# Kernel optimization log

Hardware: AMD Instinct MI355X
Metric: run time of the kernel (lower is better)

## Reference

```python
import jax, jax.numpy as jnp
import numpy as np

TI, N, TO, D, H, FF, V, L = 128, 8, 32, 512, 8, 2048, 2000, 6


def _ln(x, s, b, eps=1e-5):
    m = jnp.mean(x, -1, keepdims=True)
    v = jnp.var(x, -1, keepdims=True)
    return (x - m) / jnp.sqrt(v + eps) * s + b


def _pos_enc(t, d):
    pos = np.arange(t)[:, None]
    div = np.exp(np.arange(0, d, 2) * (-np.log(10000.0) / d))
    pe = np.zeros((t, d), np.float32)
    pe[:, 0::2] = np.sin(pos * div)
    pe[:, 1::2] = np.cos(pos * div)
    return jnp.asarray(pe)


def _forward(enc_out, embed, enc_w, enc_b, qkv_w, qkv_b, o_w, o_b, ln1_s, ln1_b,
             ff1_w, ff1_b, ff2_w, ff2_b, ln2_s, ln2_b, out_w, tgt_pad, tgt_len, sos):
    n, to = tgt_pad.shape
    t = to + 1
    v, d = embed.shape
    hd = d // H
    # prepend <sos>, embed (scaled) + sinusoidal positions; dropout omitted (eval)
    tgt = jnp.pad(tgt_pad, ((0, 0), (1, 0)), constant_values=sos)  # N x T
    x = embed[tgt] * jnp.sqrt(jnp.float32(d)) + _pos_enc(t, d)[None]  # N x T x D
    x = x.transpose(1, 0, 2)  # T x N x D (time-major, pytorch default)
    causal = jnp.triu(jnp.ones((t, t), bool), k=1)  # True = masked
    lens = jnp.maximum(tgt_len, 1)
    pad = jnp.arange(t)[None, :] >= lens[:, None]  # N x T key padding
    mask = causal[None, None] | pad[:, None, None, :]
    neg = jnp.float32(-1e9)

    def heads(z):  # T x N x D -> N x H x T x hd
        return z.reshape(t, n, H, hd).transpose(1, 2, 0, 3)

    for l in range(L):  # post-norm TransformerEncoderLayer, relu FFN
        qkv = jnp.einsum('tnd,ed->tne', x, qkv_w[l]) + qkv_b[l]
        q, k_, v_ = jnp.split(qkv, 3, axis=-1)
        q = heads(q) / jnp.sqrt(jnp.float32(hd))
        k_, v_ = heads(k_), heads(v_)
        sc = jnp.einsum('nhqd,nhkd->nhqk', q, k_)
        att = jax.nn.softmax(jnp.where(mask, neg, sc), axis=-1)
        o = jnp.einsum('nhqk,nhkd->nhqd', att, v_).transpose(2, 0, 1, 3).reshape(t, n, d)
        o = jnp.einsum('tnd,ed->tne', o, o_w[l]) + o_b[l]
        x = _ln(x + o, ln1_s[l], ln1_b[l])
        h = jax.nn.relu(jnp.einsum('tnd,fd->tnf', x, ff1_w[l]) + ff1_b[l])
        h = jnp.einsum('tnf,df->tnd', h, ff2_w[l]) + ff2_b[l]
        x = _ln(x + h, ln2_s[l], ln2_b[l])

    enc = jnp.einsum('ind,ed->ine', enc_out, enc_w) + enc_b  # Ti x N x D
    add = jnp.tanh(enc[None] + x[:, None])  # (To+1) x Ti x N x D joiner
    out = jnp.einsum('tind,vd->tinv', add, out_w)  # (To+1) x Ti x N x V
    return out.transpose(2, 1, 0, 3)  # N x Ti x (To+1) x V


def setup_inputs() -> dict:
    key = jax.random.key(0)
    ks = jax.random.split(key, 12)
    s = 0.02
    return dict(
        enc_out=jax.random.normal(ks[0], (TI, N, D), jnp.float32),
        embed=jax.random.normal(ks[1], (V, D), jnp.float32) * s,
        enc_w=jax.random.normal(ks[2], (D, D), jnp.float32) * s,
        enc_b=jnp.zeros((D,), jnp.float32),
        qkv_w=jax.random.normal(ks[3], (L, 3 * D, D), jnp.float32) * s,
        qkv_b=jnp.zeros((L, 3 * D), jnp.float32),
        o_w=jax.random.normal(ks[4], (L, D, D), jnp.float32) * s,
        o_b=jnp.zeros((L, D), jnp.float32),
        ln1_s=jnp.ones((L, D), jnp.float32),
        ln1_b=jnp.zeros((L, D), jnp.float32),
        ff1_w=jax.random.normal(ks[5], (L, FF, D), jnp.float32) * s,
        ff1_b=jnp.zeros((L, FF), jnp.float32),
        ff2_w=jax.random.normal(ks[6], (L, D, FF), jnp.float32) * s,
        ff2_b=jnp.zeros((L, D), jnp.float32),
        ln2_s=jnp.ones((L, D), jnp.float32),
        ln2_b=jnp.zeros((L, D), jnp.float32),
        out_w=jax.random.normal(ks[7], (V, D), jnp.float32) * s,
        tgt_pad=jax.random.randint(ks[8], (N, TO), 0, V),
        tgt_len=jax.random.randint(ks[9], (N,), TO // 2, TO + 2),
        sos=1,
    )


def reference(enc_out, embed, enc_w, enc_b, qkv_w, qkv_b, o_w, o_b, ln1_s, ln1_b,
              ff1_w, ff1_b, ff2_w, ff2_b, ln2_s, ln2_b, out_w, tgt_pad, tgt_len, sos):
    return _forward(enc_out, embed, enc_w, enc_b, qkv_w, qkv_b, o_w, o_b, ln1_s, ln1_b,
                    ff1_w, ff1_b, ff2_w, ff2_b, ln2_s, ln2_b, out_w, tgt_pad, tgt_len, sos)
```

## Files before the change

### kernel.cpp

```cpp
#include <hip/hip_runtime.h>
#include <hip/hip_bf16.h>
#include <math.h>

#define TI 128
#define NB 8
#define TO 32
#define TT 33
#define D 512
#define NH 8
#define HD 64
#define FF 2048
#define V 2000
#define NL 6
#define NTOK (TT*NB)
#define MJ (NB*TI*TT)
#define GRID 256

typedef __attribute__((ext_vector_type(4))) float  f4;
typedef __attribute__((ext_vector_type(8))) short  shortx8;
typedef unsigned short u16;

static constexpr size_t QO = 0;
static constexpr size_t OO = 4718592;
static constexpr size_t F1 = 6291456;
static constexpr size_t F2 = 12582912;
static constexpr size_t EW = 18874368;

__device__ __forceinline__ u16 f2bf(float f) {
    unsigned u = __float_as_uint(f);
    unsigned r = (u + 0x7fffu + ((u >> 16) & 1u)) >> 16;
    return (u16)r;
}
__device__ __forceinline__ float bf2f(u16 h) {
    return __uint_as_float(((unsigned)h) << 16);
}
__device__ __forceinline__ float wsum(float v) {
#pragma unroll
    for (int off = 32; off; off >>= 1) v += __shfl_xor(v, off, 64);
    return v;
}
__device__ __forceinline__ float wmax(float v) {
#pragma unroll
    for (int off = 32; off; off >>= 1) v = fmaxf(v, __shfl_xor(v, off, 64));
    return v;
}
__device__ __forceinline__ f4 mfma16(shortx8 a, shortx8 b, f4 c) {
    return __builtin_amdgcn_mfma_f32_16x16x32_bf16(a, b, c, 0, 0, 0);
}
__device__ __forceinline__ void async16(const void* g, void* l) {
    __builtin_amdgcn_global_load_lds(
        (const __attribute__((address_space(1))) unsigned int*)g,
        (__attribute__((address_space(3))) unsigned int*)l, 16, 0, 0);
}

__device__ __forceinline__ void grid_sync(unsigned gs, unsigned xcc, unsigned nblk,
                                          unsigned* gbar, unsigned* xarr,
                                          unsigned* xdn)
{
    __syncthreads();
    if (threadIdx.x == 0) {
        unsigned a = __hip_atomic_fetch_add(&xarr[xcc * 16], 1u, __ATOMIC_RELAXED,
                                            __HIP_MEMORY_SCOPE_AGENT);
        bool leader = (a == gs * nblk - 1);
        if (leader)
            asm volatile("buffer_wbl2 sc1\n\ts_waitcnt vmcnt(0)" ::: "memory");
        __hip_atomic_fetch_add(gbar, 1u, __ATOMIC_RELAXED, __HIP_MEMORY_SCOPE_AGENT);
        unsigned tgt = (gs + 1) * (unsigned)GRID;
        while (__hip_atomic_load(gbar, __ATOMIC_RELAXED,
                                 __HIP_MEMORY_SCOPE_AGENT) < tgt)
            __builtin_amdgcn_s_sleep(2);
        if (leader) {
            asm volatile("buffer_inv sc1\n\ts_waitcnt vmcnt(0)" ::: "memory");
            __hip_atomic_fetch_add(&xdn[xcc * 16], 1u, __ATOMIC_RELAXED,
                                   __HIP_MEMORY_SCOPE_AGENT);
        } else {
            while (__hip_atomic_load(&xdn[xcc * 16], __ATOMIC_RELAXED,
                                     __HIP_MEMORY_SCOPE_AGENT) < gs)
                __builtin_amdgcn_s_sleep(2);
            asm volatile("buffer_inv sc0\n\ts_waitcnt vmcnt(0)" ::: "memory");
        }
    }
    __syncthreads();
}

__global__ __launch_bounds__(256) void fused_convert(
    const float* __restrict__ qw, const float* __restrict__ ow,
    const float* __restrict__ f1w, const float* __restrict__ f2w,
    const float* __restrict__ ew, u16* __restrict__ Wh, u16* __restrict__ Wl,
    const float* __restrict__ enc_out, u16* __restrict__ eh, u16* __restrict__ el,
    const float* __restrict__ emb, const int* __restrict__ tgt_pad,
    const int* __restrict__ sos, float* __restrict__ x,
    u16* __restrict__ xh, u16* __restrict__ xl, unsigned* __restrict__ bar)
{
    const int bid = blockIdx.x, tid = threadIdx.x;
    if (bid == 0) { bar[tid] = 0; bar[tid + 256] = 0; }
    if (bid < 18688) {
        int i4 = bid * 256 + tid;
        const float* src; int loc;
        if (i4 < 1179648)      { src = qw;  loc = i4; }
        else if (i4 < 1572864) { src = ow;  loc = i4 - 1179648; }
        else if (i4 < 3145728) { src = f1w; loc = i4 - 1572864; }
        else if (i4 < 4718592) { src = f2w; loc = i4 - 3145728; }
        else                   { src = ew;  loc = i4 - 4718592; }
        f4 v = *(const f4*)(src + (size_t)loc * 4);
        ushort4 h, l;
        h.x = f2bf(v[0]); l.x = f2bf(v[0] - bf2f(h.x));
        h.y = f2bf(v[1]); l.y = f2bf(v[1] - bf2f(h.y));
        h.z = f2bf(v[2]); l.z = f2bf(v[2] - bf2f(h.z));
        h.w = f2bf(v[3]); l.w = f2bf(v[3] - bf2f(h.w));
        *(ushort4*)(Wh + (size_t)i4 * 4) = h;
        *(ushort4*)(Wl + (size_t)i4 * 4) = l;
    } else if (bid < 19200) {
        int i = (bid - 18688) * 256 + tid;
        f4 v = *(const f4*)(enc_out + (size_t)i * 4);
        ushort4 h, l;
        h.x = f2bf(v[0]); l.x = f2bf(v[0] - bf2f(h.x));
        h.y = f2bf(v[1]); l.y = f2bf(v[1] - bf2f(h.y));
        h.z = f2bf(v[2]); l.z = f2bf(v[2] - bf2f(h.z));
        h.w = f2bf(v[3]); l.w = f2bf(v[3] - bf2f(h.w));
        *(ushort4*)(eh + (size_t)i * 4) = h;
        *(ushort4*)(el + (size_t)i * 4) = l;
    } else {
        int idx = (bid - 19200) * 256 + tid;
        if (idx < NTOK * D) {
            int d = idx & (D - 1);
            int row = idx >> 9;
            int t = row >> 3, n = row & 7;
            int tok = (t == 0) ? *sos : tgt_pad[n * TO + t - 1];
            float freq = __expf((float)(d & ~1) * (-0.017988946039015984f));
            float ang = (float)t * freq;
            float pe = (d & 1) ? cosf(ang) : sinf(ang);
            float v = emb[tok * D + d] * 22.627416997969522f + pe;
            x[idx] = v;
            u16 h = f2bf(v);
            xh[idx] = h;
            xl[idx] = f2bf(v - bf2f(h));
        }
    }
}

template<int MODE>
__device__ void gemm_tile(
    u16 (*ls)[4][2048], int mt, int nt, int zz,
    const u16* __restrict__ Ah, const u16* __restrict__ Al, int lda,
    const u16* __restrict__ Bh, const u16* __restrict__ Bl, int ldb,
    const float* __restrict__ bias,
    float* __restrict__ C, u16* __restrict__ Ch, u16* __restrict__ Cl,
    int M, int ldc, int ksteps)
{
    const int tid = threadIdx.x, lane = tid & 63, w = tid >> 6;
    const int wr = (w >> 1) * 32, wc = (w & 1) * 32;
    const int m0 = mt * 64, n0 = nt * 64;
    const int qd = lane >> 4, mm = lane & 15;
    const int kb = (MODE == 1) ? zz * ksteps * 32 : 0;
    f4 acc[2][2] = {};
    const u16* Ab  = Ah + (size_t)m0 * lda + kb;
    const u16* Alb = Al + (size_t)m0 * lda + kb;
    const u16* Bb  = Bh + (size_t)n0 * ldb + kb;
    const u16* Blb = Bl + (size_t)n0 * ldb + kb;
    const int srow = tid >> 2;
    const int sc8  = ((tid & 3) ^ (srow & 3)) * 8;

    auto stage = [&](int b, int it) {
        int k0 = it * 32;
        async16(Ab  + (size_t)srow * lda + k0 + sc8, &ls[b][0][tid * 8]);
        async16(Alb + (size_t)srow * lda + k0 + sc8, &ls[b][1][tid * 8]);
        async16(Bb  + (size_t)srow * ldb + k0 + sc8, &ls[b][2][tid * 8]);
        async16(Blb + (size_t)srow * ldb + k0 + sc8, &ls[b][3][tid * 8]);
    };

    stage(0, 0);
    if (ksteps > 1) stage(1, 1);
    for (int it = 0; it < ksteps; ++it) {
        if (it + 1 < ksteps) asm volatile("s_waitcnt vmcnt(4)" ::: "memory");
        else                 asm volatile("s_waitcnt vmcnt(0)" ::: "memory");
        __builtin_amdgcn_s_barrier();
        if (it + 2 < ksteps) stage((it + 2) % 3, it + 2);
        const int cur = it % 3;
        shortx8 aH[2], aL[2], bH[2], bL[2];
#pragma unroll
        for (int rt = 0; rt < 2; ++rt) {
            int row = wr + rt * 16 + mm;
            int ca = (qd ^ (row & 3)) * 8;
            aH[rt] = *(const shortx8*)&ls[cur][0][row * 32 + ca];
            aL[rt] = *(const shortx8*)&ls[cur][1][row * 32 + ca];
            int col = wc + rt * 16 + mm;
            int cb = (qd ^ (col & 3)) * 8;
            bH[rt] = *(const shortx8*)&ls[cur][2][col * 32 + cb];
            bL[rt] = *(const shortx8*)&ls[cur][3][col * 32 + cb];
        }
#pragma unroll
        for (int rt = 0; rt < 2; ++rt)
#pragma unroll
            for (int ct = 0; ct < 2; ++ct) {
                acc[rt][ct] = mfma16(aH[rt], bH[ct], acc[rt][ct]);
                acc[rt][ct] = mfma16(aH[rt], bL[ct], acc[rt][ct]);
                acc[rt][ct] = mfma16(aL[rt], bH[ct], acc[rt][ct]);
            }
    }
    float* Cz = C;
    if (MODE == 1) Cz = C + (size_t)zz * (size_t)M * ldc;
#pragma unroll
    for (int rt = 0; rt < 2; ++rt)
#pragma unroll
        for (int ct = 0; ct < 2; ++ct)
#pragma unroll
            for (int reg = 0; reg < 4; ++reg) {
                int grow = m0 + wr + rt * 16 + qd * 4 + reg;
                int gcol = n0 + wc + ct * 16 + mm;
                if (grow < M) {
                    float v = acc[rt][ct][reg];
                    if (MODE != 1) v += bias[gcol];
                    if (MODE == 2) {
                        v = fmaxf(v, 0.f);
                        u16 h = f2bf(v);
                        Ch[(size_t)grow * ldc + gcol] = h;
                        Cl[(size_t)grow * ldc + gcol] = f2bf(v - bf2f(h));
                    } else {
                        Cz[(size_t)grow * ldc + gcol] = v;
                    }
                }
            }
}

__device__ void attn_body(u16* lsr, int bid,
                          const float* __restrict__ qkv,
                          const int* __restrict__ tgt_len,
                          u16* __restrict__ oh, u16* __restrict__ ol)
{
    const int n = bid >> 3, h = bid & 7;
    const int tid = threadIdx.x, lane = tid & 63, w = tid >> 6;
    float* sq  = (float*)lsr;
    float* skT = sq + TT * HD;
    float* sv  = skT + HD * TT;
    for (int idx = tid; idx < TT * HD; idx += 256) {
        int t = idx >> 6, d = idx & 63;
        size_t base = (size_t)(t * NB + n) * (3 * D) + h * HD + d;
        sq[idx] = qkv[base] * 0.125f;
        skT[d * TT + t] = qkv[base + D];
        sv[idx] = qkv[base + 2 * D];
    }
    int len = max(tgt_len[n], 1);
    __syncthreads();
    for (int r = w; r < TT; r += 4) {
        bool ok = (lane < TT) && (lane <= r) && (lane < len);
        float s = -INFINITY;
        if (ok) {
            float dot = 0.f;
#pragma unroll 8
            for (int d = 0; d < HD; ++d) dot += sq[r * HD + d] * skT[d * TT + lane];
            s = dot;
        }
        float mx = wmax(s);
        float e = ok ? __expf(s - mx) : 0.f;
        float sum = wsum(e);
        float att = e / sum;
        float o = 0.f;
#pragma unroll
        for (int k = 0; k < TT; ++k) {
            float a = __shfl(att, k, 64);
            o += a * sv[k * HD + lane];
        }
        size_t oi = (size_t)(r * NB + n) * D + h * HD + lane;
        u16 hv = f2bf(o);
        oh[oi] = hv;
        ol[oi] = f2bf(o - bf2f(hv));
    }
}

template<int NP, int BIAS>
__device__ void add_ln_body(int bid,
    float* __restrict__ x, const float* __restrict__ r,
    const float* __restrict__ bias2,
    const float* __restrict__ s, const float* __restrict__ b,
    u16* __restrict__ xh, u16* __restrict__ xl)
{
    int row = bid * 4 + (threadIdx.x >> 6);
    int lane = threadIdx.x & 63;
    if (row >= NTOK) return;
    float* xr = x + (size_t)row * D;
    f4 v1 = *(const f4*)(xr + lane * 4);
    f4 v2 = *(const f4*)(xr + 256 + lane * 4);
#pragma unroll
    for (int p = 0; p < NP; ++p) {
        const float* rr = r + (size_t)p * (NTOK * D) + (size_t)row * D;
        v1 += *(const f4*)(rr + lane * 4);
        v2 += *(const f4*)(rr + 256 + lane * 4);
    }
    if (BIAS) {
        v1 += *(const f4*)(bias2 + lane * 4);
        v2 += *(const f4*)(bias2 + 256 + lane * 4);
    }
    float sum = 0.f, sq = 0.f;
#pragma unroll
    for (int j = 0; j < 4; ++j) {
        sum += v1[j] + v2[j];
        sq += v1[j] * v1[j] + v2[j] * v2[j];
    }
    sum = wsum(sum); sq = wsum(sq);
    float mean = sum * (1.f / D);
    float var = sq * (1.f / D) - mean * mean;
    float rstd = rsqrtf(var + 1e-5f);
    f4 o1, o2;
    ushort4 h1, l1, h2, l2;
    u16 th, tl;
#pragma unroll
    for (int j = 0; j < 4; ++j) {
        int c1 = lane * 4 + j, c2 = c1 + 256;
        o1[j] = (v1[j] - mean) * rstd * s[c1] + b[c1];
        o2[j] = (v2[j] - mean) * rstd * s[c2] + b[c2];
    }
    th = f2bf(o1[0]); tl = f2bf(o1[0] - bf2f(th)); h1.x = th; l1.x = tl;
    th = f2bf(o1[1]); tl = f2bf(o1[1] - bf2f(th)); h1.y = th; l1.y = tl;
    th = f2bf(o1[2]); tl = f2bf(o1[2] - bf2f(th)); h1.z = th; l1.z = tl;
    th = f2bf(o1[3]); tl = f2bf(o1[3] - bf2f(th)); h1.w = th; l1.w = tl;
    th = f2bf(o2[0]); tl = f2bf(o2[0] - bf2f(th)); h2.x = th; l2.x = tl;
    th = f2bf(o2[1]); tl = f2bf(o2[1] - bf2f(th)); h2.y = th; l2.y = tl;
    th = f2bf(o2[2]); tl = f2bf(o2[2] - bf2f(th)); h2.z = th; l2.z = tl;
    th = f2bf(o2[3]); tl = f2bf(o2[3] - bf2f(th)); h2.w = th; l2.w = tl;
    *(f4*)(xr + lane * 4) = o1;
    *(f4*)(xr + 256 + lane * 4) = o2;
    *(ushort4*)(xh + (size_t)row * D + lane * 4) = h1;
    *(ushort4*)(xl + (size_t)row * D + lane * 4) = l1;
    *(ushort4*)(xh + (size_t)row * D + 256 + lane * 4) = h2;
    *(ushort4*)(xl + (size_t)row * D + 256 + lane * 4) = l2;
}

__global__ __launch_bounds__(256, 1) void decoder_coop(
    const u16* __restrict__ Wh, const u16* __restrict__ Wl,
    const float* __restrict__ qkv_b, const float* __restrict__ o_b,
    const float* __restrict__ ln1_s, const float* __restrict__ ln1_b,
    const float* __restrict__ ff1_b, const float* __restrict__ ff2_b,
    const float* __restrict__ ln2_s, const float* __restrict__ ln2_b,
    const float* __restrict__ enc_b, const int* __restrict__ tgt_len,
    float* __restrict__ x, float* __restrict__ qkvb,
    float* __restrict__ part, float* __restrict__ encb,
    u16* __restrict__ xh, u16* __restrict__ xl,
    u16* __restrict__ oh, u16* __restrict__ ol,
    u16* __restrict__ hh, u16* __restrict__ hl,
    const u16* __restrict__ eh, const u16* __restrict__ el,
    unsigned* __restrict__ bar)
{
    __shared__ u16 ls[3][4][2048];
    const int bid = blockIdx.x;
    const int tid = threadIdx.x;

    unsigned xcc;
    asm("s_getreg_b32 %0, hwreg(HW_REG_XCC_ID, 0, 4)" : "=s"(xcc));
    xcc &= 7;
    unsigned* gbar = bar;
    unsigned* xcnt = bar + 16;
    unsigned* xarr = bar + 144;
    unsigned* xdn  = bar + 272;

    __shared__ unsigned s_nblk;
    if (tid == 0) {
        __hip_atomic_fetch_add(&xcnt[xcc * 16], 1u, __ATOMIC_RELAXED,
                               __HIP_MEMORY_SCOPE_AGENT);
        __hip_atomic_fetch_add(gbar, 1u, __ATOMIC_RELAXED, __HIP_MEMORY_SCOPE_AGENT);
        while (__hip_atomic_load(gbar, __ATOMIC_RELAXED,
                                 __HIP_MEMORY_SCOPE_AGENT) < (unsigned)GRID)
            __builtin_amdgcn_s_sleep(2);
        s_nblk = __hip_atomic_load(&xcnt[xcc * 16], __ATOMIC_RELAXED,
                                   __HIP_MEMORY_SCOPE_AGENT);
    }
    __syncthreads();
    const unsigned nblk = s_nblk;
    unsigned gs = 0;

    const int xg = bid & 7, jg = bid >> 3;

    for (int l = 0; l < NL; ++l) {
        const u16* WqH = Wh + QO + (size_t)l * 786432;
        const u16* WqL = Wl + QO + (size_t)l * 786432;
        const u16* WoH = Wh + OO + (size_t)l * 262144;
        const u16* WoL = Wl + OO + (size_t)l * 262144;
        const u16* W1H = Wh + F1 + (size_t)l * 1048576;
        const u16* W1L = Wl + F1 + (size_t)l * 1048576;
        const u16* W2H = Wh + F2 + (size_t)l * 1048576;
        const u16* W2L = Wl + F2 + (size_t)l * 1048576;

        if (bid < 120) {
            int mt = jg % 5, nt = (jg / 5) * 8 + xg;
            gemm_tile<0>(ls, mt, nt, 0,
                         xh, xl, 512, WqH, WqL, 512,
                         qkv_b + l * 1536, qkvb, nullptr, nullptr,
                         NTOK, 1536, 16);
        } else if (l == 0 && bid < 248) {
            int t = bid - 120;
            gemm_tile<0>(ls, t >> 3, t & 7, 0,
                         eh, el, 512, Wh + EW, Wl + EW, 512,
                         enc_b, encb, nullptr, nullptr,
                         TI * NB, 512, 16);
        }
        grid_sync(++gs, xcc, nblk, gbar, xarr, xdn);

        if (bid < NB * NH) attn_body((u16*)ls, bid, qkvb, tgt_len, oh, ol);
        grid_sync(++gs, xcc, nblk, gbar, xarr, xdn);

        if (bid < 160) {
            int z = jg % 4, mt = jg / 4, nt = xg;
            gemm_tile<1>(ls, mt, nt, z,
                         oh, ol, 512, WoH, WoL, 512,
                         nullptr, part, nullptr, nullptr,
                         NTOK, 512, 4);
        }
        grid_sync(++gs, xcc, nblk, gbar, xarr, xdn);

        if (bid < 66) add_ln_body<4, 1>(bid, x, part, o_b + l * 512,
                                        ln1_s + l * 512, ln1_b + l * 512, xh, xl);
        grid_sync(++gs, xcc, nblk, gbar, xarr, xdn);

        if (bid < 160) {
            int mt = jg % 5, nt = (jg / 5) * 8 + xg;
            gemm_tile<2>(ls, mt, nt, 0,
                         xh, xl, 512, W1H, W1L, 512,
                         ff1_b + l * 2048, nullptr, hh, hl,
                         NTOK, 2048, 16);
        }
        grid_sync(++gs, xcc, nblk, gbar, xarr, xdn);

        if (bid < 160) {
            int z = jg % 4, mt = jg / 4, nt = xg;
            gemm_tile<1>(ls, mt, nt, z,
                         hh, hl, 2048, W2H, W2L, 2048,
                         nullptr, part, nullptr, nullptr,
                         NTOK, 512, 16);
        }
        grid_sync(++gs, xcc, nblk, gbar, xarr, xdn);

        if (bid < 66) add_ln_body<4, 1>(bid, x, part, ff2_b + l * 512,
                                        ln2_s + l * 512, ln2_b + l * 512, xh, xl);
        if (l < NL - 1) grid_sync(++gs, xcc, nblk, gbar, xarr, xdn);
    }
}

__global__ __launch_bounds__(256) void prep_joiner(
    const float* __restrict__ encb, const float* __restrict__ x,
    u16* __restrict__ Aj, const float* __restrict__ out_w, u16* __restrict__ Bj)
{
    const int bid = blockIdx.x;
    if (bid < 8448) {
        int idx = bid * 256 + threadIdx.x;
        int d8 = (idx & 63) << 3;
        int row = idx >> 6;
        int n = row / (TI * TT);
        int rem = row - n * (TI * TT);
        int ti = rem / TT;
        int t = rem - ti * TT;
        const float* pe = encb + (size_t)(ti * NB + n) * D + d8;
        const float* px = x + (size_t)(t * NB + n) * D + d8;
        f4 e0 = *(const f4*)pe, e1 = *(const f4*)(pe + 4);
        f4 x0 = *(const f4*)px, x1 = *(const f4*)(px + 4);
        u16* dst = Aj + (size_t)row * D + d8;
#pragma unroll
        for (int j = 0; j < 4; ++j) {
            dst[j] = f2bf(tanhf(e0[j] + x0[j]));
            dst[4 + j] = f2bf(tanhf(e1[j] + x1[j]));
        }
    } else {
        int idx = (bid - 8448) * 256 + threadIdx.x;
        int d8 = (idx & 63) << 3;
        int row = idx >> 6;
        u16* dst = Bj + (size_t)row * D + d8;
        if (row < V) {
            const float* p = out_w + (size_t)row * D + d8;
            f4 a = *(const f4*)p, b = *(const f4*)(p + 4);
#pragma unroll
            for (int j = 0; j < 4; ++j) { dst[j] = f2bf(a[j]); dst[4 + j] = f2bf(b[j]); }
        } else {
#pragma unroll
            for (int j = 0; j < 8; ++j) dst[j] = 0;
        }
    }
}

__global__ __launch_bounds__(256) void joiner_gemm(
    const u16* __restrict__ Aj, const u16* __restrict__ Bj,
    float* __restrict__ out)
{
    __shared__ u16 lsA[3][128 * 32];
    __shared__ u16 lsB[3][128 * 32];
    const int bid = blockIdx.x;
    const int v = (bid & 7) * 528 + (bid >> 3);
    const int mt = v >> 4, nt = v & 15;
    const int tid = threadIdx.x, lane = tid & 63, w = tid >> 6;
    const int wr = (w >> 1) * 64, wc = (w & 1) * 64;
    const int qd = lane >> 4, mm = lane & 15;
    f4 acc[4][4] = {};
    const u16* Abase = Aj + (size_t)mt * 128 * D;
    const u16* Bbase = Bj + (size_t)nt * 128 * D;

    auto stage = [&](int b, int it) {
        int k0 = it * 32;
#pragma unroll
        for (int i = 0; i < 2; ++i) {
            int idx = tid + i * 256;
            int row = idx >> 2, c = idx & 3;
            int chunk = c ^ ((row >> 1) & 3);
            async16(Abase + (size_t)row * D + k0 + chunk * 8, &lsA[b][idx * 8]);
            async16(Bbase + (size_t)row * D + k0 + chunk * 8, &lsB[b][idx * 8]);
        }
    };
    stage(0, 0);
    stage(1, 1);
    for (int it = 0; it < 16; ++it) {
        if (it < 15) asm volatile("s_waitcnt vmcnt(4)" ::: "memory");
        else         asm volatile("s_waitcnt vmcnt(0)" ::: "memory");
        __builtin_amdgcn_s_barrier();
        if (it + 2 < 16) stage((it + 2) % 3, it + 2);
        const int cur = it % 3;
        shortx8 af[4], bf[4];
#pragma unroll
        for (int rt = 0; rt < 4; ++rt) {
            int row = wr + rt * 16 + mm;
            int cpos = qd ^ ((row >> 1) & 3);
            af[rt] = *(const shortx8*)&lsA[cur][row * 32 + cpos * 8];
        }
#pragma unroll
        for (int ct = 0; ct < 4; ++ct) {
            int col = wc + ct * 16 + mm;
            int cpos = qd ^ ((col >> 1) & 3);
            bf[ct] = *(const shortx8*)&lsB[cur][col * 32 + cpos * 8];
        }
#pragma unroll
        for (int rt = 0; rt < 4; ++rt)
#pragma unroll
            for (int ct = 0; ct < 4; ++ct)
                acc[rt][ct] = mfma16(af[rt], bf[ct], acc[rt][ct]);
    }
#pragma unroll
    for (int rt = 0; rt < 4; ++rt)
#pragma unroll
        for (int ct = 0; ct < 4; ++ct)
#pragma unroll
            for (int reg = 0; reg < 4; ++reg) {
                int grow = mt * 128 + wr + rt * 16 + qd * 4 + reg;
                int gcol = nt * 128 + wc + ct * 16 + mm;
                if (gcol < V)
                    __builtin_nontemporal_store(acc[rt][ct][reg],
                                                &out[(size_t)grow * V + gcol]);
            }
}

extern "C" void kernel_launch(void* const* d_in, const int* in_sizes, int n_in,
                              void* d_out, int out_size, void* d_ws, size_t ws_size,
                              hipStream_t stream)
{
    const float* enc_out = (const float*)d_in[0];
    const float* embed_w = (const float*)d_in[1];
    const float* enc_w   = (const float*)d_in[2];
    const float* enc_b   = (const float*)d_in[3];
    const float* qkv_w   = (const float*)d_in[4];
    const float* qkv_b   = (const float*)d_in[5];
    const float* o_w     = (const float*)d_in[6];
    const float* o_b     = (const float*)d_in[7];
    const float* ln1_s   = (const float*)d_in[8];
    const float* ln1_b   = (const float*)d_in[9];
    const float* ff1_w   = (const float*)d_in[10];
    const float* ff1_b   = (const float*)d_in[11];
    const float* ff2_w   = (const float*)d_in[12];
    const float* ff2_b   = (const float*)d_in[13];
    const float* ln2_s   = (const float*)d_in[14];
    const float* ln2_b   = (const float*)d_in[15];
    const float* out_w   = (const float*)d_in[16];
    const int*   tgt_pad = (const int*)d_in[17];
    const int*   tgt_len = (const int*)d_in[18];
    const int*   sos     = (const int*)d_in[19];

    float* ws = (float*)d_ws;
    float* x    = ws;
    float* qkvb = ws + 135168;
    unsigned* bar = (unsigned*)(ws + 540672);
    float* part = ws + 675840;
    float* encb = ws + 1216512;
    u16* u  = (u16*)(ws + 1740800);
    u16* xh = u;                  u16* xl = xh + 320 * 512;
    u16* oh = xl + 163840;        u16* ol = oh + 163840;
    u16* hh = ol + 163840;        u16* hl = hh + 320 * 2048;
    u16* eh = hl + 655360;        u16* el = eh + 524288;
    u16* Wh = el + 524288;        u16* Wl = Wh + 19136512;
    u16* Aj = Wl + 19136512;      u16* Bj = Aj + (size_t)MJ * D;

    fused_convert<<<19728, 256, 0, stream>>>(
        qkv_w, o_w, ff1_w, ff2_w, enc_w, Wh, Wl,
        enc_out, eh, el, embed_w, tgt_pad, sos, x, xh, xl, bar);

    decoder_coop<<<GRID, 256, 0, stream>>>(
        Wh, Wl, qkv_b, o_b, ln1_s, ln1_b, ff1_b, ff2_b, ln2_s, ln2_b,
        enc_b, tgt_len, x, qkvb, part, encb,
        xh, xl, oh, ol, hh, hl, eh, el, bar);

    prep_joiner<<<8960, 256, 0, stream>>>(encb, x, Aj, out_w, Bj);

    joiner_gemm<<<264 * 16, 256, 0, stream>>>(Aj, Bj, (float*)d_out);
}
```

Baseline: 1.161 ms.

## Make grid barrier hierarchical: only per-XCC leaders touch the global counter

The grid barrier previously had all 256 blocks increment and spin on one global counter. Now only the last-arriving block of each XCC increments a second global counter and waits for all active XCCs, then releases its XCC through a per-XCC flag that the other blocks poll. This cuts traffic and contention on the global atomic across the roughly 41 barriers in the layer loop. Counters are padded further apart, the init clears more of the barrier buffer, and the startup handshake counts the active XCCs with acquire/release ordering.

```diff
diff --git a/kernel.cpp b/kernel.cpp
--- a/kernel.cpp
+++ b/kernel.cpp
@@ -54,29 +54,27 @@
 }
 
 __device__ __forceinline__ void grid_sync(unsigned gs, unsigned xcc, unsigned nblk,
-                                          unsigned* gbar, unsigned* xarr,
-                                          unsigned* xdn)
+                                          unsigned nx, unsigned* gbar2,
+                                          unsigned* xarr, unsigned* xdn)
 {
     __syncthreads();
     if (threadIdx.x == 0) {
-        unsigned a = __hip_atomic_fetch_add(&xarr[xcc * 16], 1u, __ATOMIC_RELAXED,
+        unsigned a = __hip_atomic_fetch_add(&xarr[xcc * 32], 1u, __ATOMIC_RELAXED,
                                             __HIP_MEMORY_SCOPE_AGENT);
-        bool leader = (a == gs * nblk - 1);
-        if (leader)
+        if (a == gs * nblk - 1u) {
             asm volatile("buffer_wbl2 sc1\n\ts_waitcnt vmcnt(0)" ::: "memory");
-        __hip_atomic_fetch_add(gbar, 1u, __ATOMIC_RELAXED, __HIP_MEMORY_SCOPE_AGENT);
-        unsigned tgt = (gs + 1) * (unsigned)GRID;
-        while (__hip_atomic_load(gbar, __ATOMIC_RELAXED,
-                                 __HIP_MEMORY_SCOPE_AGENT) < tgt)
-            __builtin_amdgcn_s_sleep(2);
-        if (leader) {
+            __hip_atomic_fetch_add(gbar2, 1u, __ATOMIC_RELAXED,
+                                   __HIP_MEMORY_SCOPE_AGENT);
+            while (__hip_atomic_load(gbar2, __ATOMIC_RELAXED,
+                                     __HIP_MEMORY_SCOPE_AGENT) < gs * nx)
+                __builtin_amdgcn_s_sleep(1);
             asm volatile("buffer_inv sc1\n\ts_waitcnt vmcnt(0)" ::: "memory");
-            __hip_atomic_fetch_add(&xdn[xcc * 16], 1u, __ATOMIC_RELAXED,
+            __hip_atomic_fetch_add(&xdn[xcc * 32], 1u, __ATOMIC_RELAXED,
                                    __HIP_MEMORY_SCOPE_AGENT);
         } else {
-            while (__hip_atomic_load(&xdn[xcc * 16], __ATOMIC_RELAXED,
+            while (__hip_atomic_load(&xdn[xcc * 32], __ATOMIC_RELAXED,
                                      __HIP_MEMORY_SCOPE_AGENT) < gs)
-                __builtin_amdgcn_s_sleep(2);
+                __builtin_amdgcn_s_sleep(4);
             asm volatile("buffer_inv sc0\n\ts_waitcnt vmcnt(0)" ::: "memory");
         }
     }
@@ -93,7 +91,9 @@
     u16* __restrict__ xh, u16* __restrict__ xl, unsigned* __restrict__ bar)
 {
     const int bid = blockIdx.x, tid = threadIdx.x;
-    if (bid == 0) { bar[tid] = 0; bar[tid + 256] = 0; }
+    if (bid == 0) {
+        bar[tid] = 0; bar[tid + 256] = 0; bar[tid + 512] = 0; bar[tid + 768] = 0;
+    }
     if (bid < 18688) {
         int i4 = bid * 256 + tid;
         const float* src; int loc;
@@ -348,24 +348,31 @@
     unsigned xcc;
     asm("s_getreg_b32 %0, hwreg(HW_REG_XCC_ID, 0, 4)" : "=s"(xcc));
     xcc &= 7;
-    unsigned* gbar = bar;
-    unsigned* xcnt = bar + 16;
-    unsigned* xarr = bar + 144;
-    unsigned* xdn  = bar + 272;
-
-    __shared__ unsigned s_nblk;
+    unsigned* gbar  = bar;
+    unsigned* gbar2 = bar + 16;
+    unsigned* xcnt  = bar + 64;
+    unsigned* xarr  = bar + 320;
+    unsigned* xdn   = bar + 576;
+
+    __shared__ unsigned s_nblk, s_nx;
     if (tid == 0) {
-        __hip_atomic_fetch_add(&xcnt[xcc * 16], 1u, __ATOMIC_RELAXED,
+        __hip_atomic_fetch_add(&xcnt[xcc * 32], 1u, __ATOMIC_ACQ_REL,
                                __HIP_MEMORY_SCOPE_AGENT);
-        __hip_atomic_fetch_add(gbar, 1u, __ATOMIC_RELAXED, __HIP_MEMORY_SCOPE_AGENT);
-        while (__hip_atomic_load(gbar, __ATOMIC_RELAXED,
+        __hip_atomic_fetch_add(gbar, 1u, __ATOMIC_ACQ_REL, __HIP_MEMORY_SCOPE_AGENT);
+        while (__hip_atomic_load(gbar, __ATOMIC_ACQUIRE,
                                  __HIP_MEMORY_SCOPE_AGENT) < (unsigned)GRID)
             __builtin_amdgcn_s_sleep(2);
-        s_nblk = __hip_atomic_load(&xcnt[xcc * 16], __ATOMIC_RELAXED,
+        s_nblk = __hip_atomic_load(&xcnt[xcc * 32], __ATOMIC_ACQUIRE,
                                    __HIP_MEMORY_SCOPE_AGENT);
+        unsigned nx = 0;
+#pragma unroll
+        for (int i = 0; i < 8; ++i)
+            nx += (__hip_atomic_load(&xcnt[i * 32], __ATOMIC_ACQUIRE,
+                                     __HIP_MEMORY_SCOPE_AGENT) != 0u);
+        s_nx = nx;
     }
     __syncthreads();
-    const unsigned nblk = s_nblk;
+    const unsigned nblk = s_nblk, nx = s_nx;
     unsigned gs = 0;
 
     const int xg = bid & 7, jg = bid >> 3;
@@ -393,10 +400,10 @@
                          enc_b, encb, nullptr, nullptr,
                          TI * NB, 512, 16);
         }
-        grid_sync(++gs, xcc, nblk, gbar, xarr, xdn);
+        grid_sync(++gs, xcc, nblk, nx, gbar2, xarr, xdn);
 
         if (bid < NB * NH) attn_body((u16*)ls, bid, qkvb, tgt_len, oh, ol);
-        grid_sync(++gs, xcc, nblk, gbar, xarr, xdn);
+        grid_sync(++gs, xcc, nblk, nx, gbar2, xarr, xdn);
 
         if (bid < 160) {
             int z = jg % 4, mt = jg / 4, nt = xg;
@@ -405,11 +412,11 @@
                          nullptr, part, nullptr, nullptr,
                          NTOK, 512, 4);
         }
-        grid_sync(++gs, xcc, nblk, gbar, xarr, xdn);
+        grid_sync(++gs, xcc, nblk, nx, gbar2, xarr, xdn);
 
         if (bid < 66) add_ln_body<4, 1>(bid, x, part, o_b + l * 512,
                                         ln1_s + l * 512, ln1_b + l * 512, xh, xl);
-        grid_sync(++gs, xcc, nblk, gbar, xarr, xdn);
+        grid_sync(++gs, xcc, nblk, nx, gbar2, xarr, xdn);
 
         if (bid < 160) {
             int mt = jg % 5, nt = (jg / 5) * 8 + xg;
@@ -418,7 +425,7 @@
                          ff1_b + l * 2048, nullptr, hh, hl,
                          NTOK, 2048, 16);
         }
-        grid_sync(++gs, xcc, nblk, gbar, xarr, xdn);
+        grid_sync(++gs, xcc, nblk, nx, gbar2, xarr, xdn);
 
         if (bid < 160) {
             int z = jg % 4, mt = jg / 4, nt = xg;
@@ -427,11 +434,11 @@
                          nullptr, part, nullptr, nullptr,
                          NTOK, 512, 16);
         }
-        grid_sync(++gs, xcc, nblk, gbar, xarr, xdn);
+        grid_sync(++gs, xcc, nblk, nx, gbar2, xarr, xdn);
 
         if (bid < 66) add_ln_body<4, 1>(bid, x, part, ff2_b + l * 512,
                                         ln2_s + l * 512, ln2_b + l * 512, xh, xl);
-        if (l < NL - 1) grid_sync(++gs, xcc, nblk, gbar, xarr, xdn);
+        if (l < NL - 1) grid_sync(++gs, xcc, nblk, nx, gbar2, xarr, xdn);
     }
 }
 
```

New measurement: 964.4 us. 1.2x faster.
